# Kernel tuning notes

Measured on AMD Instinct MI355X. Metric: run time of the kernel, lower is better.

## Reference

```python
import jax, jax.numpy as jnp
import numpy as np

C = 32            # channels per irrep (32x0e + 32x1o)
N = 50000         # nodes
E = 800000        # edges (avg degree 16)
INV_SQRT_C = 1.0 / np.sqrt(C).astype(np.float32)
INV_SQRT_3 = 1.0 / np.sqrt(3.0).astype(np.float32)


def _lin_s(s, w):
    # per-irrep channel-mixing linear on scalars: [n,C] @ [C,C]
    return (s @ w) * INV_SQRT_C


def _lin_v(v, w):
    # channel-mixing linear on l=1 vectors (acts on channel dim only, equivariant)
    return jnp.einsum('ncx,cd->ndx', v, w) * INV_SQRT_C


def resblock(s, v, w):
    # w: [7,C,C] = lin1_s, lin1_v, gate, lin2_s, lin2_v, skip_s, skip_v
    # Lin -> gated nonlinearity (silu on scalars, scalar-gated vectors) -> Lin, plus linear skip.
    s1 = _lin_s(s, w[0])
    v1 = _lin_v(v, w[1])
    g = jax.nn.sigmoid(_lin_s(s1, w[2]))          # equivariant gates from scalars
    s2 = jax.nn.silu(s1)
    v2 = v1 * g[..., None]
    s_out = _lin_s(s2, w[3]) + _lin_s(s, w[5])
    v_out = _lin_v(v2, w[4]) + _lin_v(v, w[6])
    return s_out, v_out


def tp_uvu(sl, vl, sr, vr, w):
    # 'uvu' irreps tensor product for 32x0e+32x1o x 32x0e+32x1o -> 32x0e+32x1o
    # 4 CG paths, weights w: [4,C,C]; output channel index = left channel (u).
    # 0e (x) 0e -> 0e
    sr0 = jnp.einsum('nv,uv->nu', sr, w[0]) * INV_SQRT_C
    # 1o (x) 1o -> 0e  (dot product CG, coeff 1/sqrt(3)); fold weight into right first
    vr1 = jnp.einsum('nvx,uv->nux', vr, w[1]) * INV_SQRT_C
    s_out = sl * sr0 + jnp.sum(vl * vr1, axis=-1) * INV_SQRT_3
    # 0e (x) 1o -> 1o
    vr2 = jnp.einsum('nvx,uv->nux', vr, w[2]) * INV_SQRT_C
    # 1o (x) 0e -> 1o
    sr3 = jnp.einsum('nv,uv->nu', sr, w[3]) * INV_SQRT_C
    v_out = sl[..., None] * vr2 + vl * sr3[..., None]
    return s_out, v_out


def setup_inputs() -> dict:
    key = jax.random.key(0)
    k1, k2, k3, k4, k5 = jax.random.split(key, 5)
    node_s = jax.random.normal(k1, (N, C), dtype=jnp.float32)
    node_v = jax.random.normal(k2, (N, C, 3), dtype=jnp.float32)
    tp_w = jax.random.normal(k3, (2, 4, C, C), dtype=jnp.float32)
    res_w = jax.random.normal(k4, (6, 7, C, C), dtype=jnp.float32)
    edge_index = jax.random.randint(k5, (2, E), 0, N, dtype=jnp.int64)
    return {'node_s': node_s, 'node_v': node_v, 'tp_w': tp_w,
            'res_w': res_w, 'edge_index': edge_index}


def reference(node_s, node_v, tp_w, res_w, edge_index):
    src, dst = edge_index[0], edge_index[1]
    # --- off-diagonal (per-edge) branch ---
    nb_s, nb_v = node_s[src], node_v[src]          # neighbor = node_features[src]
    ce_s, ce_v = node_s[dst], node_v[dst]          # center   = node_features[dst]
    cs, cv = resblock(ce_s, ce_v, res_w[0])        # res_center_off
    off_s, off_v = tp_uvu(cs, cv, nb_s, nb_v, tp_w[1])   # tp_off
    off_s, off_v = resblock(off_s, off_v, res_w[1])      # res_pair_off
    rs, rv = resblock(ce_s, ce_v, res_w[2])               # res_res_off
    off_s, off_v = rs + off_s, rv + off_v
    # --- diagonal (per-node) branch ---
    ds, dv = resblock(node_s, node_v, res_w[3])    # res_center
    dg_s, dg_v = tp_uvu(ds, dv, node_s, node_v, tp_w[0])  # tp
    dg_s, dg_v = resblock(dg_s, dg_v, res_w[4])            # res_pair
    qs, qv = resblock(node_s, node_v, res_w[5])            # res_res
    dg_s, dg_v = qs + dg_s, qv + dg_v
    return dg_s, dg_v, off_s, off_v
```

## Files before the change

kernel.cpp:

```cpp
#include <hip/hip_runtime.h>
#include <hip/hip_bf16.h>

#define DEV __device__ __forceinline__

typedef unsigned short u16;
typedef unsigned int u32;

typedef __attribute__((ext_vector_type(8))) short bf16x8;
typedef __attribute__((ext_vector_type(4))) float f32x4;

constexpr float INV_C  = 0.17677669529663687f;
constexpr float INV_S3 = 0.5773502691896258f;

DEV float bf2f(u32 h) { return __uint_as_float(h << 16); }
DEV u32 f2bf_bits(float f) {
  u32 u = __float_as_uint(f);
  u += 0x7fffu + ((u >> 16) & 1u);
  return u >> 16;
}

DEV void st32f(float* __restrict__ p, const float o[32]) {
#pragma unroll
  for (int i = 0; i < 8; ++i) {
    float4 q; q.x=o[4*i+0]; q.y=o[4*i+1]; q.z=o[4*i+2]; q.w=o[4*i+3];
    reinterpret_cast<float4*>(p)[i] = q;
  }
}
DEV void ld32h(const u16* __restrict__ p, float o[32]) {
#pragma unroll
  for (int i = 0; i < 4; ++i) {
    uint4 q = reinterpret_cast<const uint4*>(p)[i];
    u32 w0=q.x, w1=q.y, w2=q.z, w3=q.w;
    o[8*i+0]=bf2f(w0 & 0xffffu); o[8*i+1]=bf2f(w0 >> 16);
    o[8*i+2]=bf2f(w1 & 0xffffu); o[8*i+3]=bf2f(w1 >> 16);
    o[8*i+4]=bf2f(w2 & 0xffffu); o[8*i+5]=bf2f(w2 >> 16);
    o[8*i+6]=bf2f(w3 & 0xffffu); o[8*i+7]=bf2f(w3 >> 16);
  }
}
DEV void st32h(u16* __restrict__ p, const float o[32]) {
#pragma unroll
  for (int i = 0; i < 16; ++i) {
    reinterpret_cast<u32*>(p)[i] = f2bf_bits(o[2*i]) | (f2bf_bits(o[2*i+1]) << 16);
  }
}
DEV void ld8h(const u16* __restrict__ p, float o[8]) {
  uint4 q = *reinterpret_cast<const uint4*>(p);
  o[0]=bf2f(q.x & 0xffffu); o[1]=bf2f(q.x >> 16);
  o[2]=bf2f(q.y & 0xffffu); o[3]=bf2f(q.y >> 16);
  o[4]=bf2f(q.z & 0xffffu); o[5]=bf2f(q.z >> 16);
  o[6]=bf2f(q.w & 0xffffu); o[7]=bf2f(q.w >> 16);
}
DEV bf16x8 cvt8(const float t[8]) {
  bf16x8 r;
#pragma unroll
  for (int j = 0; j < 8; ++j) r[j] = (short)f2bf_bits(t[j]);
  return r;
}

DEV f32x4 mfma16(bf16x8 a, bf16x8 b, f32x4 c) {
  return __builtin_amdgcn_mfma_f32_16x16x32_bf16(a, b, c, 0, 0, 0);
}

DEV bf16x8 ldBfrag(const float* __restrict__ W, int kg, int colbase) {
  bf16x8 r;
#pragma unroll
  for (int j = 0; j < 8; ++j)
    r[j] = (short)f2bf_bits(W[(kg*8 + j)*32 + colbase]);
  return r;
}
DEV bf16x8 ldBfragT(const float* __restrict__ W, int kg, int colbase) {
  bf16x8 r;
  const float* p = W + colbase*32 + kg*8;
#pragma unroll
  for (int j = 0; j < 8; ++j) r[j] = (short)f2bf_bits(p[j]);
  return r;
}

DEV float sigmoidf(float x) { return 1.f / (1.f + __expf(-x)); }

DEV void mfma_resblock(const float* __restrict__ W7, const bf16x8 tA[4],
                       int col, int kg, float* wbuf, f32x4 co[8]) {
  const f32x4 zero4 = {0.f,0.f,0.f,0.f};
  bf16x8 B1s[2], B1v[2], Bg[2], B2s[2], B2v[2], Bks[2], Bkv[2];
#pragma unroll
  for (int ct = 0; ct < 2; ++ct) {
    int cb = ct*16 + col;
    B1s[ct] = ldBfrag(W7 + 0*1024, kg, cb);
    B1v[ct] = ldBfrag(W7 + 1*1024, kg, cb);
    Bg[ct]  = ldBfrag(W7 + 2*1024, kg, cb);
    B2s[ct] = ldBfrag(W7 + 3*1024, kg, cb);
    B2v[ct] = ldBfrag(W7 + 4*1024, kg, cb);
    Bks[ct] = ldBfrag(W7 + 5*1024, kg, cb);
    Bkv[ct] = ldBfrag(W7 + 6*1024, kg, cb);
  }
  f32x4 c1[8];
#pragma unroll
  for (int i = 0; i < 8; ++i) { c1[i] = zero4; co[i] = zero4; }
#pragma unroll
  for (int rt = 0; rt < 4; ++rt)
#pragma unroll
    for (int ct = 0; ct < 2; ++ct) {
      c1[rt*2+ct] = mfma16(tA[rt], rt==0 ? B1s[ct] : B1v[ct], c1[rt*2+ct]);
      co[rt*2+ct] = mfma16(tA[rt], rt==0 ? Bks[ct] : Bkv[ct], co[rt*2+ct]);
    }
#pragma unroll
  for (int i = 0; i < 8; ++i) c1[i] *= INV_C;

#pragma unroll
  for (int ct = 0; ct < 2; ++ct)
#pragma unroll
    for (int i = 0; i < 4; ++i)
      wbuf[(kg*4 + i)*36 + ct*16 + col] = c1[ct][i];
  float ag[8];
  *reinterpret_cast<float4*>(&ag[0]) = *reinterpret_cast<const float4*>(&wbuf[col*36 + kg*8]);
  *reinterpret_cast<float4*>(&ag[4]) = *reinterpret_cast<const float4*>(&wbuf[col*36 + kg*8 + 4]);
  bf16x8 Ag = cvt8(ag);
  f32x4 cg0 = mfma16(Ag, Bg[0], zero4);
  f32x4 cg1 = mfma16(Ag, Bg[1], zero4);
  float g0[4], g1[4];
#pragma unroll
  for (int i = 0; i < 4; ++i) {
    g0[i] = sigmoidf(cg0[i]*INV_C);
    g1[i] = sigmoidf(cg1[i]*INV_C);
  }

#pragma unroll
  for (int ct = 0; ct < 2; ++ct)
#pragma unroll
    for (int i = 0; i < 4; ++i) {
      float v = c1[ct][i];
      c1[ct][i] = v * sigmoidf(v);
    }
#pragma unroll
  for (int rt = 1; rt < 4; ++rt)
#pragma unroll
    for (int ct = 0; ct < 2; ++ct)
#pragma unroll
      for (int i = 0; i < 4; ++i)
        c1[rt*2+ct][i] *= (ct == 0 ? g0[i] : g1[i]);

#pragma unroll
  for (int rt = 0; rt < 4; ++rt)
#pragma unroll
    for (int ct = 0; ct < 2; ++ct)
#pragma unroll
      for (int i = 0; i < 4; ++i)
        wbuf[(rt*16 + kg*4 + i)*36 + ct*16 + col] = c1[rt*2+ct][i];
  bf16x8 t2A[4];
#pragma unroll
  for (int rt = 0; rt < 4; ++rt) {
    float a8[8];
    *reinterpret_cast<float4*>(&a8[0]) = *reinterpret_cast<const float4*>(&wbuf[(rt*16+col)*36 + kg*8]);
    *reinterpret_cast<float4*>(&a8[4]) = *reinterpret_cast<const float4*>(&wbuf[(rt*16+col)*36 + kg*8 + 4]);
    t2A[rt] = cvt8(a8);
  }

#pragma unroll
  for (int rt = 0; rt < 4; ++rt)
#pragma unroll
    for (int ct = 0; ct < 2; ++ct)
      co[rt*2+ct] = mfma16(t2A[rt], rt==0 ? B2s[ct] : B2v[ct], co[rt*2+ct]);
#pragma unroll
  for (int i = 0; i < 8; ++i) co[i] *= INV_C;
}


__global__ __launch_bounds__(256) void nodeA_kernel(
    const float* __restrict__ node_s, const float* __restrict__ node_v,
    const float* __restrict__ tpw, const float* __restrict__ resw,
    u16* __restrict__ wsN, int N, int ntN)
{
  __shared__ __align__(16) float sbuf[9216];
  const int lane = threadIdx.x & 63;
  const int wave = threadIdx.x >> 6;
  float* wbuf = sbuf + wave*2304;
  const int col = lane & 15;
  const int kg  = lane >> 4;

  const int task = blockIdx.x*4 + wave;
  const int job  = task / ntN;
  const int tile = task - job*ntN;
  if (job >= 6) return;

  const int n0 = tile*16 + col;
  const int nc = (n0 < N) ? n0 : (N-1);
  bf16x8 fA[4];
  {
    float t[8];
    const float* ps = node_s + (size_t)nc*32 + kg*8;
#pragma unroll
    for (int j = 0; j < 8; ++j) t[j] = ps[j];
    fA[0] = cvt8(t);
    const float* pv = node_v + (size_t)nc*96 + kg*24;
#pragma unroll
    for (int x = 0; x < 3; ++x) {
      float tv[8];
#pragma unroll
      for (int j = 0; j < 8; ++j) tv[j] = pv[j*3 + x];
      fA[x+1] = cvt8(tv);
    }
  }

  const int eloc = lane >> 2, comp = lane & 3;
  const int n2 = tile*16 + eloc;

  if (job < 4) {
    const int rbi  = (job==0) ? 0 : (job==1) ? 2 : (job==2) ? 3 : 5;
    const int ooff = (job==0) ? 0 : (job==1) ? 128 : (job==2) ? 512 : 640;
    f32x4 co[8];
    mfma_resblock(resw + rbi*7168, fA, col, kg, wbuf, co);
#pragma unroll
    for (int rt = 0; rt < 4; ++rt)
#pragma unroll
      for (int ct = 0; ct < 2; ++ct)
#pragma unroll
        for (int i = 0; i < 4; ++i)
          wbuf[(rt*16 + kg*4 + i)*33 + ct*16 + col] = co[rt*2+ct][i];
    if (n2 < N) {
      float o[32];
      const float* rp = &wbuf[(comp*16 + eloc)*33];
#pragma unroll
      for (int m = 0; m < 32; ++m) o[m] = rp[m];
      st32h(wsN + (size_t)n2*1024 + ooff + comp*32, o);
    }
  } else {
    const float* Wt = (job==4) ? tpw + 4096 : tpw;
    bf16x8 Bw[4][2];
#pragma unroll
    for (int m = 0; m < 4; ++m)
#pragma unroll
      for (int ct = 0; ct < 2; ++ct)
        Bw[m][ct] = ldBfragT(Wt + m*1024, kg, ct*16 + col);
    const int base1  = (job==4) ? 256 : 768;
    const int base2v = (job==4) ? 384 : 896;
    const int base2s = (job==4) ? 480 : 992;
    const f32x4 zero4 = {0.f,0.f,0.f,0.f};
    {
      f32x4 c[8];
#pragma unroll
      for (int i = 0; i < 8; ++i) c[i] = zero4;
#pragma unroll
      for (int rt = 0; rt < 4; ++rt)
#pragma unroll
        for (int ct = 0; ct < 2; ++ct)
          c[rt*2+ct] = mfma16(fA[rt], rt==0 ? Bw[0][ct] : Bw[1][ct], c[rt*2+ct]);
#pragma unroll
      for (int rt = 0; rt < 4; ++rt)
#pragma unroll
        for (int ct = 0; ct < 2; ++ct)
#pragma unroll
          for (int i = 0; i < 4; ++i)
            wbuf[(rt*16 + kg*4 + i)*33 + ct*16 + col] = c[rt*2+ct][i]*INV_C;
      if (n2 < N) {
        float o[32];
        const float* rp = &wbuf[(comp*16 + eloc)*33];
#pragma unroll
        for (int m = 0; m < 32; ++m) o[m] = rp[m];
        st32h(wsN + (size_t)n2*1024 + base1 + comp*32, o);
      }
    }
    {
      f32x4 c[8];
#pragma unroll
      for (int i = 0; i < 8; ++i) c[i] = zero4;
#pragma unroll
      for (int rt = 0; rt < 4; ++rt)
#pragma unroll
        for (int ct = 0; ct < 2; ++ct)
          c[rt*2+ct] = mfma16(fA[rt], rt==0 ? Bw[3][ct] : Bw[2][ct], c[rt*2+ct]);
#pragma unroll
      for (int rt = 0; rt < 4; ++rt)
#pragma unroll
        for (int ct = 0; ct < 2; ++ct)
#pragma unroll
          for (int i = 0; i < 4; ++i)
            wbuf[(rt*16 + kg*4 + i)*33 + ct*16 + col] = c[rt*2+ct][i]*INV_C;
      if (n2 < N) {
        float o[32];
        const float* rp = &wbuf[(comp*16 + eloc)*33];
#pragma unroll
        for (int m = 0; m < 32; ++m) o[m] = rp[m];
        const int off = (comp==0) ? base2s : base2v + 32*(comp-1);
        st32h(wsN + (size_t)n2*1024 + off, o);
      }
    }
  }
}

__global__ __launch_bounds__(256) void nodeB_kernel(
    const u16* __restrict__ wsN, const float* __restrict__ resw,
    float* __restrict__ dgs, float* __restrict__ dgv, int N, int ntN)
{
  __shared__ __align__(16) float sbuf[9216];
  const int lane = threadIdx.x & 63;
  const int wave = threadIdx.x >> 6;
  float* wbuf = sbuf + wave*2304;
  const int col = lane & 15;
  const int kg  = lane >> 4;

  const int tile = blockIdx.x*4 + wave;
  if (tile >= ntN) return;

  const int n0 = tile*16 + col;
  const int nc = (n0 < N) ? n0 : (N-1);
  const u16* P = wsN + (size_t)nc*1024 + kg*8;

  float DSs[8], DSv0[8], DSv1[8], DSv2[8], b[8], acc[8], t[8];
  ld8h(P + 512, DSs);
  ld8h(P + 544, DSv0);
  ld8h(P + 576, DSv1);
  ld8h(P + 608, DSv2);

  bf16x8 tA[4];
  ld8h(P + 768, b);
#pragma unroll
  for (int j = 0; j < 8; ++j) t[j] = DSs[j]*b[j];
  ld8h(P + 800, b);
#pragma unroll
  for (int j = 0; j < 8; ++j) acc[j] = DSv0[j]*b[j];
  ld8h(P + 832, b);
#pragma unroll
  for (int j = 0; j < 8; ++j) acc[j] = __builtin_fmaf(DSv1[j], b[j], acc[j]);
  ld8h(P + 864, b);
#pragma unroll
  for (int j = 0; j < 8; ++j) acc[j] = __builtin_fmaf(DSv2[j], b[j], acc[j]);
#pragma unroll
  for (int j = 0; j < 8; ++j) t[j] = __builtin_fmaf(acc[j], INV_S3, t[j]);
  tA[0] = cvt8(t);

  float sr3[8];
  ld8h(P + 992, sr3);
  ld8h(P + 896, b);
#pragma unroll
  for (int j = 0; j < 8; ++j) t[j] = DSs[j]*b[j] + DSv0[j]*sr3[j];
  tA[1] = cvt8(t);
  ld8h(P + 928, b);
#pragma unroll
  for (int j = 0; j < 8; ++j) t[j] = DSs[j]*b[j] + DSv1[j]*sr3[j];
  tA[2] = cvt8(t);
  ld8h(P + 960, b);
#pragma unroll
  for (int j = 0; j < 8; ++j) t[j] = DSs[j]*b[j] + DSv2[j]*sr3[j];
  tA[3] = cvt8(t);

  f32x4 co[8];
  mfma_resblock(resw + 4*7168, tA, col, kg, wbuf, co);

#pragma unroll
  for (int rt = 0; rt < 4; ++rt)
#pragma unroll
    for (int ct = 0; ct < 2; ++ct)
#pragma unroll
      for (int i = 0; i < 4; ++i)
        wbuf[(rt*16 + kg*4 + i)*33 + ct*16 + col] = co[rt*2+ct][i];

  const int eloc = lane >> 2, comp = lane & 3;
  const int n2 = tile*16 + eloc;
  const int nc2 = (n2 < N) ? n2 : (N-1);
  float o[32];
  {
    const float* rp = &wbuf[(comp*16 + eloc)*33];
#pragma unroll
    for (int m = 0; m < 32; ++m) o[m] = rp[m];
  }
  {
    float q[32];
    ld32h(wsN + (size_t)nc2*1024 + 640 + comp*32, q);
#pragma unroll
    for (int c = 0; c < 32; ++c) o[c] += q[c];
  }
  if (comp == 0) {
    if (n2 < N) st32f(dgs + (size_t)n2*32, o);
  } else {
#pragma unroll
    for (int c = 0; c < 32; ++c) wbuf[eloc*97 + 3*c + (comp-1)] = o[c];
  }
  {
    const size_t obase = (size_t)tile * 1536;
#pragma unroll
    for (int i = 0; i < 6; ++i) {
      int s = i*64 + lane;
      int row = s / 24, c4 = s - row*24;
      const float* sp = &wbuf[row*97 + c4*4];
      float4 q; q.x = sp[0]; q.y = sp[1]; q.z = sp[2]; q.w = sp[3];
      if (tile*16 + row < N)
        *reinterpret_cast<float4*>(dgv + obase + (size_t)s*4) = q;
    }
  }
}

__global__ __launch_bounds__(256) void edge_kernel(
    const int* __restrict__ ei, const float* __restrict__ resw,
    const u16* __restrict__ wsN,
    float* __restrict__ offs, float* __restrict__ offv, int E, int ntiles)
{
  __shared__ __align__(16) float sbuf[9216];
  const int lane = threadIdx.x & 63;
  const int wave = threadIdx.x >> 6;
  float* wbuf = sbuf + wave*2304;

  const int col = lane & 15;
  const int kg  = lane >> 4;

  const float* W = resw + 7168;
  bf16x8 Bs1[2], Bv1[2], Bg[2], Bl2s[2], Bl2v[2], Bsks[2], Bskv[2];
#pragma unroll
  for (int ct = 0; ct < 2; ++ct) {
    int cb = ct*16 + col;
    Bs1[ct]  = ldBfrag(W + 0*1024, kg, cb);
    Bv1[ct]  = ldBfrag(W + 1*1024, kg, cb);
    Bg[ct]   = ldBfrag(W + 2*1024, kg, cb);
    Bl2s[ct] = ldBfrag(W + 3*1024, kg, cb);
    Bl2v[ct] = ldBfrag(W + 4*1024, kg, cb);
    Bsks[ct] = ldBfrag(W + 5*1024, kg, cb);
    Bskv[ct] = ldBfrag(W + 6*1024, kg, cb);
  }

  const int wid = blockIdx.x*4 + wave;
  const int wstride = gridDim.x*4;
  const f32x4 zero4 = {0.f, 0.f, 0.f, 0.f};

  for (int tile = wid; tile < ntiles; tile += wstride) {
    int e = tile*16 + col;
    int ec = (e < E) ? e : (E - 1);
    int sn = ei[ec], dn = ei[(size_t)E + ec];
    const u16* S = wsN + (size_t)sn*1024 + kg*8;
    const u16* D = wsN + (size_t)dn*1024 + kg*8;

    float As[8], Av0[8], Av1[8], Av2[8], b[8], acc[8], t[8];
    ld8h(D + 0,  As);
    ld8h(D + 32, Av0);
    ld8h(D + 64, Av1);
    ld8h(D + 96, Av2);

    bf16x8 tA[4];
    ld8h(S + 256, b);
#pragma unroll
    for (int j = 0; j < 8; ++j) t[j] = As[j]*b[j];
    ld8h(S + 288, b);
#pragma unroll
    for (int j = 0; j < 8; ++j) acc[j] = Av0[j]*b[j];
    ld8h(S + 320, b);
#pragma unroll
    for (int j = 0; j < 8; ++j) acc[j] = __builtin_fmaf(Av1[j], b[j], acc[j]);
    ld8h(S + 352, b);
#pragma unroll
    for (int j = 0; j < 8; ++j) acc[j] = __builtin_fmaf(Av2[j], b[j], acc[j]);
#pragma unroll
    for (int j = 0; j < 8; ++j) t[j] = __builtin_fmaf(acc[j], INV_S3, t[j]);
    tA[0] = cvt8(t);

    ld8h(S + 480, acc);
    ld8h(S + 384, b);
#pragma unroll
    for (int j = 0; j < 8; ++j) t[j] = As[j]*b[j] + Av0[j]*acc[j];
    tA[1] = cvt8(t);
    ld8h(S + 416, b);
#pragma unroll
    for (int j = 0; j < 8; ++j) t[j] = As[j]*b[j] + Av1[j]*acc[j];
    tA[2] = cvt8(t);
    ld8h(S + 448, b);
#pragma unroll
    for (int j = 0; j < 8; ++j) t[j] = As[j]*b[j] + Av2[j]*acc[j];
    tA[3] = cvt8(t);

    f32x4 c1[8], co[8];
#pragma unroll
    for (int i = 0; i < 8; ++i) { c1[i] = zero4; co[i] = zero4; }
#pragma unroll
    for (int rt = 0; rt < 4; ++rt) {
#pragma unroll
      for (int ct = 0; ct < 2; ++ct) {
        c1[rt*2+ct] = mfma16(tA[rt], rt==0 ? Bs1[ct] : Bv1[ct], c1[rt*2+ct]);
        co[rt*2+ct] = mfma16(tA[rt], rt==0 ? Bsks[ct] : Bskv[ct], co[rt*2+ct]);
      }
    }
#pragma unroll
    for (int i = 0; i < 8; ++i) c1[i] *= INV_C;

#pragma unroll
    for (int ct = 0; ct < 2; ++ct)
#pragma unroll
      for (int i = 0; i < 4; ++i)
        wbuf[(kg*4 + i)*36 + ct*16 + col] = c1[ct][i];
    float ag[8];
    *reinterpret_cast<float4*>(&ag[0]) = *reinterpret_cast<const float4*>(&wbuf[col*36 + kg*8]);
    *reinterpret_cast<float4*>(&ag[4]) = *reinterpret_cast<const float4*>(&wbuf[col*36 + kg*8 + 4]);
    bf16x8 Ag = cvt8(ag);
    f32x4 cg0 = mfma16(Ag, Bg[0], zero4);
    f32x4 cg1 = mfma16(Ag, Bg[1], zero4);
    float g0[4], g1[4];
#pragma unroll
    for (int i = 0; i < 4; ++i) {
      g0[i] = sigmoidf(cg0[i]*INV_C);
      g1[i] = sigmoidf(cg1[i]*INV_C);
    }

#pragma unroll
    for (int ct = 0; ct < 2; ++ct)
#pragma unroll
      for (int i = 0; i < 4; ++i) {
        float v = c1[ct][i];
        c1[ct][i] = v * sigmoidf(v);
      }
#pragma unroll
    for (int rt = 1; rt < 4; ++rt)
#pragma unroll
      for (int ct = 0; ct < 2; ++ct)
#pragma unroll
        for (int i = 0; i < 4; ++i)
          c1[rt*2+ct][i] *= (ct == 0 ? g0[i] : g1[i]);

#pragma unroll
    for (int rt = 0; rt < 4; ++rt)
#pragma unroll
      for (int ct = 0; ct < 2; ++ct)
#pragma unroll
        for (int i = 0; i < 4; ++i)
          wbuf[(rt*16 + kg*4 + i)*36 + ct*16 + col] = c1[rt*2+ct][i];
    bf16x8 t2A[4];
#pragma unroll
    for (int rt = 0; rt < 4; ++rt) {
      float a8[8];
      *reinterpret_cast<float4*>(&a8[0]) = *reinterpret_cast<const float4*>(&wbuf[(rt*16+col)*36 + kg*8]);
      *reinterpret_cast<float4*>(&a8[4]) = *reinterpret_cast<const float4*>(&wbuf[(rt*16+col)*36 + kg*8 + 4]);
      t2A[rt] = cvt8(a8);
    }

#pragma unroll
    for (int rt = 0; rt < 4; ++rt)
#pragma unroll
      for (int ct = 0; ct < 2; ++ct)
        co[rt*2+ct] = mfma16(t2A[rt], rt==0 ? Bl2s[ct] : Bl2v[ct], co[rt*2+ct]);
#pragma unroll
    for (int i = 0; i < 8; ++i) co[i] *= INV_C;

#pragma unroll
    for (int rt = 0; rt < 4; ++rt)
#pragma unroll
      for (int ct = 0; ct < 2; ++ct)
#pragma unroll
        for (int i = 0; i < 4; ++i)
          wbuf[(rt*16 + kg*4 + i)*33 + ct*16 + col] = co[rt*2+ct][i];

    const int eloc = lane >> 2, comp = lane & 3;
    float o[32];
    {
      const float* rp = &wbuf[(comp*16 + eloc)*33];
#pragma unroll
      for (int m = 0; m < 32; ++m) o[m] = rp[m];
    }
    int e2 = tile*16 + eloc;
    int ec2 = (e2 < E) ? e2 : (E - 1);
    int dn2 = ei[(size_t)E + ec2];
    {
      float r[32];
      ld32h(wsN + (size_t)dn2*1024 + 128 + comp*32, r);
#pragma unroll
      for (int c = 0; c < 32; ++c) o[c] += r[c];
    }
    if (comp == 0) {
      if (e2 < E) st32f(offs + (size_t)e2*32, o);
    } else {
#pragma unroll
      for (int c = 0; c < 32; ++c) wbuf[eloc*97 + 3*c + (comp-1)] = o[c];
    }
    {
      const size_t obase = (size_t)tile * 1536;
#pragma unroll
      for (int i = 0; i < 6; ++i) {
        int s = i*64 + lane;
        int row = s / 24, c4 = s - row*24;
        const float* sp = &wbuf[row*97 + c4*4];
        float4 q; q.x = sp[0]; q.y = sp[1]; q.z = sp[2]; q.w = sp[3];
        if (tile*16 + row < E)
          *reinterpret_cast<float4*>(offv + obase + (size_t)s*4) = q;
      }
    }
  }
}

extern "C" void kernel_launch(void* const* d_in, const int* in_sizes, int n_in,
                              void* d_out, int out_size, void* d_ws, size_t ws_size,
                              hipStream_t stream) {
  const float* node_s = (const float*)d_in[0];
  const float* node_v = (const float*)d_in[1];
  const float* tpw    = (const float*)d_in[2];
  const float* resw   = (const float*)d_in[3];
  const int*   ei     = (const int*)d_in[4];
  const int N = in_sizes[0] / 32;
  const int E = in_sizes[4] / 2;

  float* out  = (float*)d_out;
  float* dgs  = out;
  float* dgv  = out + (size_t)N*32;
  float* offs = out + (size_t)N*128;
  float* offv = offs + (size_t)E*32;

  u16* wsB = (u16*)d_ws;

  const int ntN = (N + 15) / 16;
  const int ntE = (E + 15) / 16;

  const int aBlocks = (6*ntN + 3) / 4;
  const int bBlocks = (ntN + 3) / 4;
  int eg = (ntE + 3) / 4; if (eg > 2048) eg = 2048;

  nodeA_kernel<<<aBlocks, 256, 0, stream>>>(node_s, node_v, tpw, resw, wsB, N, ntN);
  nodeB_kernel<<<bBlocks, 256, 0, stream>>>(wsB, resw, dgs, dgv, N, ntN);
  edge_kernel<<<eg, 256, 0, stream>>>(ei, resw, wsB, offs, offv, E, ntE);
}
```

Before: 338.6 us.

## Split node workspace, fuse nodeB into edge kernel, prefetch next tile gathers

```diff
diff --git a/kernel.cpp b/kernel.cpp
--- a/kernel.cpp
+++ b/kernel.cpp
@@ -43,13 +43,15 @@
     reinterpret_cast<u32*>(p)[i] = f2bf_bits(o[2*i]) | (f2bf_bits(o[2*i+1]) << 16);
   }
 }
-DEV void ld8h(const u16* __restrict__ p, float o[8]) {
-  uint4 q = *reinterpret_cast<const uint4*>(p);
+DEV void cv8(uint4 q, float o[8]) {
   o[0]=bf2f(q.x & 0xffffu); o[1]=bf2f(q.x >> 16);
   o[2]=bf2f(q.y & 0xffffu); o[3]=bf2f(q.y >> 16);
   o[4]=bf2f(q.z & 0xffffu); o[5]=bf2f(q.z >> 16);
   o[6]=bf2f(q.w & 0xffffu); o[7]=bf2f(q.w >> 16);
 }
+DEV void ld8h(const u16* __restrict__ p, float o[8]) {
+  cv8(*reinterpret_cast<const uint4*>(p), o);
+}
 DEV bf16x8 cvt8(const float t[8]) {
   bf16x8 r;
 #pragma unroll
@@ -65,14 +67,14 @@
   bf16x8 r;
 #pragma unroll
   for (int j = 0; j < 8; ++j)
-    r[j] = (short)f2bf_bits(W[(kg*8 + j)*32 + colbase]);
+    r[j] = (short)f2bf_bits(W[(kg*8 + j)*32 + colbase] * INV_C);
   return r;
 }
 DEV bf16x8 ldBfragT(const float* __restrict__ W, int kg, int colbase) {
   bf16x8 r;
   const float* p = W + colbase*32 + kg*8;
 #pragma unroll
-  for (int j = 0; j < 8; ++j) r[j] = (short)f2bf_bits(p[j]);
+  for (int j = 0; j < 8; ++j) r[j] = (short)f2bf_bits(p[j] * INV_C);
   return r;
 }
 
@@ -103,8 +105,6 @@
       c1[rt*2+ct] = mfma16(tA[rt], rt==0 ? B1s[ct] : B1v[ct], c1[rt*2+ct]);
       co[rt*2+ct] = mfma16(tA[rt], rt==0 ? Bks[ct] : Bkv[ct], co[rt*2+ct]);
     }
-#pragma unroll
-  for (int i = 0; i < 8; ++i) c1[i] *= INV_C;
 
 #pragma unroll
   for (int ct = 0; ct < 2; ++ct)
@@ -120,8 +120,8 @@
   float g0[4], g1[4];
 #pragma unroll
   for (int i = 0; i < 4; ++i) {
-    g0[i] = sigmoidf(cg0[i]*INV_C);
-    g1[i] = sigmoidf(cg1[i]*INV_C);
+    g0[i] = sigmoidf(cg0[i]);
+    g1[i] = sigmoidf(cg1[i]);
   }
 
 #pragma unroll
@@ -160,15 +160,13 @@
 #pragma unroll
     for (int ct = 0; ct < 2; ++ct)
       co[rt*2+ct] = mfma16(t2A[rt], rt==0 ? B2s[ct] : B2v[ct], co[rt*2+ct]);
-#pragma unroll
-  for (int i = 0; i < 8; ++i) co[i] *= INV_C;
 }
 
 
 __global__ __launch_bounds__(256) void nodeA_kernel(
     const float* __restrict__ node_s, const float* __restrict__ node_v,
     const float* __restrict__ tpw, const float* __restrict__ resw,
-    u16* __restrict__ wsN, int N, int ntN)
+    u16* __restrict__ wsE, u16* __restrict__ wsD, int N, int ntN)
 {
   __shared__ __align__(16) float sbuf[9216];
   const int lane = threadIdx.x & 63;
@@ -206,7 +204,8 @@
 
   if (job < 4) {
     const int rbi  = (job==0) ? 0 : (job==1) ? 2 : (job==2) ? 3 : 5;
-    const int ooff = (job==0) ? 0 : (job==1) ? 128 : (job==2) ? 512 : 640;
+    u16* bp = (job < 2) ? wsE : wsD;
+    const int ooff = ((job & 1) == 0) ? 0 : 128;
     f32x4 co[8];
     mfma_resblock(resw + rbi*7168, fA, col, kg, wbuf, co);
 #pragma unroll
@@ -221,19 +220,17 @@
       const float* rp = &wbuf[(comp*16 + eloc)*33];
 #pragma unroll
       for (int m = 0; m < 32; ++m) o[m] = rp[m];
-      st32h(wsN + (size_t)n2*1024 + ooff + comp*32, o);
+      st32h(bp + (size_t)n2*512 + ooff + comp*32, o);
     }
   } else {
     const float* Wt = (job==4) ? tpw + 4096 : tpw;
+    u16* bp = (job==4) ? wsE : wsD;
     bf16x8 Bw[4][2];
 #pragma unroll
     for (int m = 0; m < 4; ++m)
 #pragma unroll
       for (int ct = 0; ct < 2; ++ct)
         Bw[m][ct] = ldBfragT(Wt + m*1024, kg, ct*16 + col);
-    const int base1  = (job==4) ? 256 : 768;
-    const int base2v = (job==4) ? 384 : 896;
-    const int base2s = (job==4) ? 480 : 992;
     const f32x4 zero4 = {0.f,0.f,0.f,0.f};
     {
       f32x4 c[8];
@@ -250,13 +247,13 @@
         for (int ct = 0; ct < 2; ++ct)
 #pragma unroll
           for (int i = 0; i < 4; ++i)
-            wbuf[(rt*16 + kg*4 + i)*33 + ct*16 + col] = c[rt*2+ct][i]*INV_C;
+            wbuf[(rt*16 + kg*4 + i)*33 + ct*16 + col] = c[rt*2+ct][i];
       if (n2 < N) {
         float o[32];
         const float* rp = &wbuf[(comp*16 + eloc)*33];
 #pragma unroll
         for (int m = 0; m < 32; ++m) o[m] = rp[m];
-        st32h(wsN + (size_t)n2*1024 + base1 + comp*32, o);
+        st32h(bp + (size_t)n2*512 + 256 + comp*32, o);
       }
     }
     {
@@ -274,22 +271,25 @@
         for (int ct = 0; ct < 2; ++ct)
 #pragma unroll
           for (int i = 0; i < 4; ++i)
-            wbuf[(rt*16 + kg*4 + i)*33 + ct*16 + col] = c[rt*2+ct][i]*INV_C;
+            wbuf[(rt*16 + kg*4 + i)*33 + ct*16 + col] = c[rt*2+ct][i];
       if (n2 < N) {
         float o[32];
         const float* rp = &wbuf[(comp*16 + eloc)*33];
 #pragma unroll
         for (int m = 0; m < 32; ++m) o[m] = rp[m];
-        const int off = (comp==0) ? base2s : base2v + 32*(comp-1);
-        st32h(wsN + (size_t)n2*1024 + off, o);
+        const int off = (comp==0) ? 480 : 384 + 32*(comp-1);
+        st32h(bp + (size_t)n2*512 + off, o);
       }
     }
   }
 }
 
-__global__ __launch_bounds__(256) void nodeB_kernel(
-    const u16* __restrict__ wsN, const float* __restrict__ resw,
-    float* __restrict__ dgs, float* __restrict__ dgv, int N, int ntN)
+__global__ __launch_bounds__(256) void edgeB_kernel(
+    const int* __restrict__ ei, const float* __restrict__ resw,
+    const u16* __restrict__ wsE, const u16* __restrict__ wsD,
+    float* __restrict__ offs, float* __restrict__ offv,
+    float* __restrict__ dgs, float* __restrict__ dgv,
+    int E, int ntE, int N, int ntN, int egB)
 {
   __shared__ __align__(16) float sbuf[9216];
   const int lane = threadIdx.x & 63;
@@ -297,110 +297,99 @@
   float* wbuf = sbuf + wave*2304;
   const int col = lane & 15;
   const int kg  = lane >> 4;
-
-  const int tile = blockIdx.x*4 + wave;
-  if (tile >= ntN) return;
-
-  const int n0 = tile*16 + col;
-  const int nc = (n0 < N) ? n0 : (N-1);
-  const u16* P = wsN + (size_t)nc*1024 + kg*8;
-
-  float DSs[8], DSv0[8], DSv1[8], DSv2[8], b[8], acc[8], t[8];
-  ld8h(P + 512, DSs);
-  ld8h(P + 544, DSv0);
-  ld8h(P + 576, DSv1);
-  ld8h(P + 608, DSv2);
-
-  bf16x8 tA[4];
-  ld8h(P + 768, b);
-#pragma unroll
-  for (int j = 0; j < 8; ++j) t[j] = DSs[j]*b[j];
-  ld8h(P + 800, b);
-#pragma unroll
-  for (int j = 0; j < 8; ++j) acc[j] = DSv0[j]*b[j];
-  ld8h(P + 832, b);
-#pragma unroll
-  for (int j = 0; j < 8; ++j) acc[j] = __builtin_fmaf(DSv1[j], b[j], acc[j]);
-  ld8h(P + 864, b);
-#pragma unroll
-  for (int j = 0; j < 8; ++j) acc[j] = __builtin_fmaf(DSv2[j], b[j], acc[j]);
-#pragma unroll
-  for (int j = 0; j < 8; ++j) t[j] = __builtin_fmaf(acc[j], INV_S3, t[j]);
-  tA[0] = cvt8(t);
-
-  float sr3[8];
-  ld8h(P + 992, sr3);
-  ld8h(P + 896, b);
-#pragma unroll
-  for (int j = 0; j < 8; ++j) t[j] = DSs[j]*b[j] + DSv0[j]*sr3[j];
-  tA[1] = cvt8(t);
-  ld8h(P + 928, b);
-#pragma unroll
-  for (int j = 0; j < 8; ++j) t[j] = DSs[j]*b[j] + DSv1[j]*sr3[j];
-  tA[2] = cvt8(t);
-  ld8h(P + 960, b);
-#pragma unroll
-  for (int j = 0; j < 8; ++j) t[j] = DSs[j]*b[j] + DSv2[j]*sr3[j];
-  tA[3] = cvt8(t);
-
-  f32x4 co[8];
-  mfma_resblock(resw + 4*7168, tA, col, kg, wbuf, co);
-
-#pragma unroll
-  for (int rt = 0; rt < 4; ++rt)
-#pragma unroll
-    for (int ct = 0; ct < 2; ++ct)
-#pragma unroll
-      for (int i = 0; i < 4; ++i)
-        wbuf[(rt*16 + kg*4 + i)*33 + ct*16 + col] = co[rt*2+ct][i];
-
-  const int eloc = lane >> 2, comp = lane & 3;
-  const int n2 = tile*16 + eloc;
-  const int nc2 = (n2 < N) ? n2 : (N-1);
-  float o[32];
-  {
-    const float* rp = &wbuf[(comp*16 + eloc)*33];
-#pragma unroll
-    for (int m = 0; m < 32; ++m) o[m] = rp[m];
-  }
-  {
-    float q[32];
-    ld32h(wsN + (size_t)nc2*1024 + 640 + comp*32, q);
-#pragma unroll
-    for (int c = 0; c < 32; ++c) o[c] += q[c];
-  }
-  if (comp == 0) {
-    if (n2 < N) st32f(dgs + (size_t)n2*32, o);
-  } else {
-#pragma unroll
-    for (int c = 0; c < 32; ++c) wbuf[eloc*97 + 3*c + (comp-1)] = o[c];
-  }
-  {
-    const size_t obase = (size_t)tile * 1536;
-#pragma unroll
-    for (int i = 0; i < 6; ++i) {
-      int s = i*64 + lane;
-      int row = s / 24, c4 = s - row*24;
-      const float* sp = &wbuf[row*97 + c4*4];
-      float4 q; q.x = sp[0]; q.y = sp[1]; q.z = sp[2]; q.w = sp[3];
-      if (tile*16 + row < N)
-        *reinterpret_cast<float4*>(dgv + obase + (size_t)s*4) = q;
-    }
-  }
-}
-
-__global__ __launch_bounds__(256) void edge_kernel(
-    const int* __restrict__ ei, const float* __restrict__ resw,
-    const u16* __restrict__ wsN,
-    float* __restrict__ offs, float* __restrict__ offv, int E, int ntiles)
-{
-  __shared__ __align__(16) float sbuf[9216];
-  const int lane = threadIdx.x & 63;
-  const int wave = threadIdx.x >> 6;
-  float* wbuf = sbuf + wave*2304;
-
-  const int col = lane & 15;
-  const int kg  = lane >> 4;
+  const f32x4 zero4 = {0.f, 0.f, 0.f, 0.f};
+
+  if ((int)blockIdx.x >= egB) {
+    const int tile = ((int)blockIdx.x - egB)*4 + wave;
+    if (tile >= ntN) return;
+    const int n0 = tile*16 + col;
+    const int nc = (n0 < N) ? n0 : (N-1);
+    const u16* P = wsD + (size_t)nc*512 + kg*8;
+
+    float DSs[8], DSv0[8], DSv1[8], DSv2[8], b[8], acc[8], t[8];
+    ld8h(P + 0,  DSs);
+    ld8h(P + 32, DSv0);
+    ld8h(P + 64, DSv1);
+    ld8h(P + 96, DSv2);
+
+    bf16x8 tA[4];
+    ld8h(P + 256, b);
+#pragma unroll
+    for (int j = 0; j < 8; ++j) t[j] = DSs[j]*b[j];
+    ld8h(P + 288, b);
+#pragma unroll
+    for (int j = 0; j < 8; ++j) acc[j] = DSv0[j]*b[j];
+    ld8h(P + 320, b);
+#pragma unroll
+    for (int j = 0; j < 8; ++j) acc[j] = __builtin_fmaf(DSv1[j], b[j], acc[j]);
+    ld8h(P + 352, b);
+#pragma unroll
+    for (int j = 0; j < 8; ++j) acc[j] = __builtin_fmaf(DSv2[j], b[j], acc[j]);
+#pragma unroll
+    for (int j = 0; j < 8; ++j) t[j] = __builtin_fmaf(acc[j], INV_S3, t[j]);
+    tA[0] = cvt8(t);
+
+    float sr3[8];
+    ld8h(P + 480, sr3);
+    ld8h(P + 384, b);
+#pragma unroll
+    for (int j = 0; j < 8; ++j) t[j] = DSs[j]*b[j] + DSv0[j]*sr3[j];
+    tA[1] = cvt8(t);
+    ld8h(P + 416, b);
+#pragma unroll
+    for (int j = 0; j < 8; ++j) t[j] = DSs[j]*b[j] + DSv1[j]*sr3[j];
+    tA[2] = cvt8(t);
+    ld8h(P + 448, b);
+#pragma unroll
+    for (int j = 0; j < 8; ++j) t[j] = DSs[j]*b[j] + DSv2[j]*sr3[j];
+    tA[3] = cvt8(t);
+
+    f32x4 co[8];
+    mfma_resblock(resw + 4*7168, tA, col, kg, wbuf, co);
+
+#pragma unroll
+    for (int rt = 0; rt < 4; ++rt)
+#pragma unroll
+      for (int ct = 0; ct < 2; ++ct)
+#pragma unroll
+        for (int i = 0; i < 4; ++i)
+          wbuf[(rt*16 + kg*4 + i)*33 + ct*16 + col] = co[rt*2+ct][i];
+
+    const int eloc = lane >> 2, comp = lane & 3;
+    const int n2 = tile*16 + eloc;
+    const int nc2 = (n2 < N) ? n2 : (N-1);
+    float o[32];
+    {
+      const float* rp = &wbuf[(comp*16 + eloc)*33];
+#pragma unroll
+      for (int m = 0; m < 32; ++m) o[m] = rp[m];
+    }
+    {
+      float q[32];
+      ld32h(wsD + (size_t)nc2*512 + 128 + comp*32, q);
+#pragma unroll
+      for (int c = 0; c < 32; ++c) o[c] += q[c];
+    }
+    if (comp == 0) {
+      if (n2 < N) st32f(dgs + (size_t)n2*32, o);
+    } else {
+#pragma unroll
+      for (int c = 0; c < 32; ++c) wbuf[eloc*97 + 3*c + (comp-1)] = o[c];
+    }
+    {
+      const size_t obase = (size_t)tile * 1536;
+#pragma unroll
+      for (int i = 0; i < 6; ++i) {
+        int s = i*64 + lane;
+        int row = s / 24, c4 = s - row*24;
+        const float* sp = &wbuf[row*97 + c4*4];
+        float4 q; q.x = sp[0]; q.y = sp[1]; q.z = sp[2]; q.w = sp[3];
+        if (tile*16 + row < N)
+          *reinterpret_cast<float4*>(dgv + obase + (size_t)s*4) = q;
+      }
+    }
+    return;
+  }
 
   const float* W = resw + 7168;
   bf16x8 Bs1[2], Bv1[2], Bg[2], Bl2s[2], Bl2v[2], Bsks[2], Bskv[2];
@@ -416,23 +405,44 @@
     Bskv[ct] = ldBfrag(W + 6*1024, kg, cb);
   }
 
-  const int wid = blockIdx.x*4 + wave;
-  const int wstride = gridDim.x*4;
-  const f32x4 zero4 = {0.f, 0.f, 0.f, 0.f};
-
-  for (int tile = wid; tile < ntiles; tile += wstride) {
+  const int wstride = egB*4;
+  int tile = blockIdx.x*4 + wave;
+  if (tile >= ntE) return;
+
+  int sn_n, dn_n;
+  uint4 dA0, dA1, dA2, dA3;
+  {
     int e = tile*16 + col;
-    int ec = (e < E) ? e : (E - 1);
-    int sn = ei[ec], dn = ei[(size_t)E + ec];
-    const u16* S = wsN + (size_t)sn*1024 + kg*8;
-    const u16* D = wsN + (size_t)dn*1024 + kg*8;
+    int ec = (e < E) ? e : (E-1);
+    sn_n = ei[ec]; dn_n = ei[(size_t)E + ec];
+    const u16* Dp = wsE + (size_t)dn_n*512 + kg*8;
+    dA0 = *reinterpret_cast<const uint4*>(Dp +  0);
+    dA1 = *reinterpret_cast<const uint4*>(Dp + 32);
+    dA2 = *reinterpret_cast<const uint4*>(Dp + 64);
+    dA3 = *reinterpret_cast<const uint4*>(Dp + 96);
+  }
+
+  for (;;) {
+    const int ctile = tile;
+    const int sn = sn_n;
+    uint4 cA0 = dA0, cA1 = dA1, cA2 = dA2, cA3 = dA3;
+
+    tile += wstride;
+    if (tile < ntE) {
+      int e = tile*16 + col;
+      int ec = (e < E) ? e : (E-1);
+      sn_n = ei[ec]; dn_n = ei[(size_t)E + ec];
+      const u16* Dp = wsE + (size_t)dn_n*512 + kg*8;
+      dA0 = *reinterpret_cast<const uint4*>(Dp +  0);
+      dA1 = *reinterpret_cast<const uint4*>(Dp + 32);
+      dA2 = *reinterpret_cast<const uint4*>(Dp + 64);
+      dA3 = *reinterpret_cast<const uint4*>(Dp + 96);
+    }
 
     float As[8], Av0[8], Av1[8], Av2[8], b[8], acc[8], t[8];
-    ld8h(D + 0,  As);
-    ld8h(D + 32, Av0);
-    ld8h(D + 64, Av1);
-    ld8h(D + 96, Av2);
-
+    cv8(cA0, As); cv8(cA1, Av0); cv8(cA2, Av1); cv8(cA3, Av2);
+
+    const u16* S = wsE + (size_t)sn*512 + kg*8;
     bf16x8 tA[4];
     ld8h(S + 256, b);
 #pragma unroll
@@ -475,8 +485,6 @@
         co[rt*2+ct] = mfma16(tA[rt], rt==0 ? Bsks[ct] : Bskv[ct], co[rt*2+ct]);
       }
     }
-#pragma unroll
-    for (int i = 0; i < 8; ++i) c1[i] *= INV_C;
 
 #pragma unroll
     for (int ct = 0; ct < 2; ++ct)
@@ -492,8 +500,8 @@
     float g0[4], g1[4];
 #pragma unroll
     for (int i = 0; i < 4; ++i) {
-      g0[i] = sigmoidf(cg0[i]*INV_C);
-      g1[i] = sigmoidf(cg1[i]*INV_C);
+      g0[i] = sigmoidf(cg0[i]);
+      g1[i] = sigmoidf(cg1[i]);
     }
 
 #pragma unroll
@@ -532,8 +540,6 @@
 #pragma unroll
       for (int ct = 0; ct < 2; ++ct)
         co[rt*2+ct] = mfma16(t2A[rt], rt==0 ? Bl2s[ct] : Bl2v[ct], co[rt*2+ct]);
-#pragma unroll
-    for (int i = 0; i < 8; ++i) co[i] *= INV_C;
 
 #pragma unroll
     for (int rt = 0; rt < 4; ++rt)
@@ -550,12 +556,12 @@
 #pragma unroll
       for (int m = 0; m < 32; ++m) o[m] = rp[m];
     }
-    int e2 = tile*16 + eloc;
+    int e2 = ctile*16 + eloc;
     int ec2 = (e2 < E) ? e2 : (E - 1);
     int dn2 = ei[(size_t)E + ec2];
     {
       float r[32];
-      ld32h(wsN + (size_t)dn2*1024 + 128 + comp*32, r);
+      ld32h(wsE + (size_t)dn2*512 + 128 + comp*32, r);
 #pragma unroll
       for (int c = 0; c < 32; ++c) o[c] += r[c];
     }
@@ -566,17 +572,19 @@
       for (int c = 0; c < 32; ++c) wbuf[eloc*97 + 3*c + (comp-1)] = o[c];
     }
     {
-      const size_t obase = (size_t)tile * 1536;
+      const size_t obase = (size_t)ctile * 1536;
 #pragma unroll
       for (int i = 0; i < 6; ++i) {
         int s = i*64 + lane;
         int row = s / 24, c4 = s - row*24;
         const float* sp = &wbuf[row*97 + c4*4];
         float4 q; q.x = sp[0]; q.y = sp[1]; q.z = sp[2]; q.w = sp[3];
-        if (tile*16 + row < E)
+        if (ctile*16 + row < E)
           *reinterpret_cast<float4*>(offv + obase + (size_t)s*4) = q;
       }
     }
+
+    if (tile >= ntE) break;
   }
 }
 
@@ -597,16 +605,19 @@
   float* offs = out + (size_t)N*128;
   float* offv = offs + (size_t)E*32;
 
-  u16* wsB = (u16*)d_ws;
+  u16* wsE = (u16*)d_ws;
+  u16* wsD = wsE + (size_t)N*512;
 
   const int ntN = (N + 15) / 16;
   const int ntE = (E + 15) / 16;
 
   const int aBlocks = (6*ntN + 3) / 4;
   const int bBlocks = (ntN + 3) / 4;
-  int eg = (ntE + 3) / 4; if (eg > 2048) eg = 2048;
-
-  nodeA_kernel<<<aBlocks, 256, 0, stream>>>(node_s, node_v, tpw, resw, wsB, N, ntN);
-  nodeB_kernel<<<bBlocks, 256, 0, stream>>>(wsB, resw, dgs, dgv, N, ntN);
-  edge_kernel<<<eg, 256, 0, stream>>>(ei, resw, wsB, offs, offv, E, ntE);
-}
+  int egB = (ntE + 3) / 4; if (egB > 4096) egB = 4096;
+
+  nodeA_kernel<<<aBlocks, 256, 0, stream>>>(node_s, node_v, tpw, resw,
+                                            wsE, wsD, N, ntN);
+  edgeB_kernel<<<egB + bBlocks, 256, 0, stream>>>(ei, resw, wsE, wsD,
+                                                  offs, offv, dgs, dgv,
+                                                  E, ntE, N, ntN, egB);
+}
```

New measurement: 302.1 us. -10.8%, faster.
